# Kernel tuning notes

Hardware: AMD Instinct MI355X
Metric: run time of the kernel (lower is better)

The kernel has to match this reference:

```python
import jax, jax.numpy as jnp
import numpy as np

B, C, H, W, K, NCLASS = 8, 512, 96, 96, 32, 19
EPS = 1e-5


def setup_inputs() -> dict:
    key = jax.random.key(0)
    ks = jax.random.split(key, 10)
    return {
        "x": jax.random.normal(ks[0], (B, C, H, W), dtype=jnp.float32),
        "conv_w": jax.random.normal(ks[1], (C, C), dtype=jnp.float32) * (1.0 / np.sqrt(C)),
        "bn2_w": jax.random.uniform(ks[2], (C,), dtype=jnp.float32, minval=0.5, maxval=1.5),
        "bn2_b": jax.random.normal(ks[3], (C,), dtype=jnp.float32) * 0.1,
        "bn2_mean": jnp.zeros((C,), jnp.float32),
        "bn2_var": jnp.ones((C,), jnp.float32),
        "codewords": jax.random.normal(ks[4], (K, C), dtype=jnp.float32) * (1.0 / np.sqrt(C)),
        "scale": jax.random.uniform(ks[5], (K,), dtype=jnp.float32, minval=-1.0, maxval=0.0),
        "bn1_w": jax.random.uniform(ks[6], (K,), dtype=jnp.float32, minval=0.5, maxval=1.5),
        "bn1_b": jax.random.normal(ks[7], (K,), dtype=jnp.float32) * 0.1,
        "bn1_mean": jnp.zeros((K,), jnp.float32),
        "bn1_var": jnp.ones((K,), jnp.float32),
        "fc_w": jax.random.normal(ks[8], (C, C), dtype=jnp.float32) * (1.0 / np.sqrt(C)),
        "fc_b": jnp.zeros((C,), jnp.float32),
        "se_w": jax.random.normal(ks[9], (NCLASS, C), dtype=jnp.float32) * (1.0 / np.sqrt(C)),
        "se_b": jnp.zeros((NCLASS,), jnp.float32),
    }


def reference(x, conv_w, bn2_w, bn2_b, bn2_mean, bn2_var,
              codewords, scale, bn1_w, bn1_b, bn1_mean, bn1_var,
              fc_w, fc_b, se_w, se_b):
    # 1x1 conv (no bias) + BN2d (inference) + ReLU
    h = jnp.einsum('oc,bchw->bohw', conv_w, x)
    s2 = bn2_w / jnp.sqrt(bn2_var + EPS)
    h = jax.nn.relu(h * s2[None, :, None, None]
                    + (bn2_b - bn2_mean * s2)[None, :, None, None])

    # Encoding: soft assignment over K codewords
    X = h.reshape(B, C, H * W).transpose(0, 2, 1)       # (B, N, C)
    x2 = jnp.sum(X * X, axis=-1)                        # (B, N)
    c2 = jnp.sum(codewords * codewords, axis=-1)        # (K,)
    xc = jnp.einsum('bnd,kd->bnk', X, codewords)        # (B, N, K)
    sl = scale[None, None, :] * (x2[:, :, None] - 2.0 * xc + c2[None, None, :])
    A = jax.nn.softmax(sl, axis=-1)                     # (B, N, K)
    # E[b,k,d] = sum_n A[b,n,k] * (X[b,n,d] - codewords[k,d])
    E = (jnp.einsum('bnk,bnd->bkd', A, X)
         - jnp.sum(A, axis=1)[:, :, None] * codewords[None, :, :])  # (B, K, C)

    # BN1d over the K channel dim (inference) + ReLU + mean over K
    s1 = bn1_w / jnp.sqrt(bn1_var + EPS)
    E = jax.nn.relu(E * s1[None, :, None] + (bn1_b - bn1_mean * s1)[None, :, None])
    en = jnp.mean(E, axis=1)                            # (B, C)

    # SE-style gate
    gamma = jax.nn.sigmoid(en @ fc_w.T + fc_b)          # (B, C)
    out = jax.nn.relu(x + x * gamma[:, :, None, None])  # (B, C, H, W)
    se = en @ se_w.T + se_b                             # (B, NCLASS)
    return (out, se)
```

## Files before the change

### kernel.cpp

```cpp
#include <hip/hip_runtime.h>
#include <math.h>

#define EPSV 1e-5f

typedef __attribute__((ext_vector_type(8))) short short8;
typedef __attribute__((ext_vector_type(4))) float f32x4;

namespace {
constexpr int NB=8, C=512, NPIX=9216, K=32, NCLS=19;

constexpr size_t o_WB    = 0;
constexpr size_t o_CWB   = 131072;
constexpr size_t o_A2    = 139264;
constexpr size_t o_B2    = 139776;
constexpr size_t o_C2    = 140288;
constexpr size_t o_X2    = 140320;
constexpr size_t o_EW    = 214048;
constexpr size_t o_ACNT  = 345120;
constexpr size_t o_EN    = 345376;
constexpr size_t o_GAMMA = 349472;
constexpr size_t o_XT    = 353568;
constexpr size_t o_EPART = 19227936;
constexpr size_t WS_NEED = (o_EPART + (size_t)384*16384) * 4;

constexpr int NGRP   = 48;
constexpr int NTILE  = 3;
constexpr int ZERO_FL = NB*C*K + 256;
constexpr int CONV_LDS = (512*64 + 64*64)*2 + 64*4;
constexpr int ENC_LDS  = 36864*2 + 2304*2 + 64*4;
}

__device__ __forceinline__ ushort f2bf(float f){
  unsigned u = __float_as_uint(f);
  return (ushort)((u + 0x7FFFu + ((u>>16)&1u)) >> 16);
}
__device__ __forceinline__ float bf2f(ushort h){
  return __uint_as_float(((unsigned)h)<<16);
}

__global__ __launch_bounds__(256) void k_prep(
    const float* __restrict__ convw, ushort* __restrict__ Wb,
    const float* __restrict__ cw,    ushort* __restrict__ cwb,
    const float* __restrict__ bn2w, const float* __restrict__ bn2b,
    const float* __restrict__ bn2m, const float* __restrict__ bn2v,
    float* __restrict__ pa, float* __restrict__ pb, float* __restrict__ c2g,
    float* __restrict__ zero_dst)
{
  const int bid = blockIdx.x, t = threadIdx.x;
  if (bid < 136){
    const float* src = (bid < 128) ? convw : cw;
    ushort* dst      = (bid < 128) ? Wb    : cwb;
    const int base   = (bid < 128) ? bid   : (bid - 128);
    int i = (base*256 + t)*8;
    float4 a = *(const float4*)(src+i), b = *(const float4*)(src+i+4);
    uint4 o;
    o.x = f2bf(a.x) | ((unsigned)f2bf(a.y)<<16);
    o.y = f2bf(a.z) | ((unsigned)f2bf(a.w)<<16);
    o.z = f2bf(b.x) | ((unsigned)f2bf(b.y)<<16);
    o.w = f2bf(b.z) | ((unsigned)f2bf(b.w)<<16);
    *(uint4*)(dst+i) = o;
  } else if (bid == 136){
    for (int o = t; o < C; o += 256){
      float s = bn2w[o] * rsqrtf(bn2v[o] + EPSV);
      pa[o] = s;
      pb[o] = bn2b[o] - bn2m[o] * s;
    }
    int kk = t>>3, part = t&7;
    float s = 0.f;
    for (int c = part*64; c < part*64 + 64; c += 4){
      float4 w = *(const float4*)(cw + kk*512 + c);
      s += w.x*w.x + w.y*w.y + w.z*w.z + w.w*w.w;
    }
    s += __shfl_xor(s, 1);
    s += __shfl_xor(s, 2);
    s += __shfl_xor(s, 4);
    if (part == 0) c2g[kk] = s;
  } else {
    const int idx = ((bid - 137)*256 + t)*4;
    if (idx < ZERO_FL)
      *(float4*)(zero_dst + idx) = make_float4(0.f, 0.f, 0.f, 0.f);
  }
}

__global__ __launch_bounds__(256) void k_T(const float* __restrict__ x,
                                           ushort* __restrict__ xT){
  __shared__ float xs[64*68];
  const int bid = blockIdx.x;
  const int ct = bid & 7;
  const int nt = bid >> 3;
  const int b = nt / 144, ntl = nt % 144;
  const int c0 = ct*64, n0 = ntl*64;
  const int t = threadIdx.x;
  const float* src = x + ((size_t)b*C + c0)*NPIX + n0;
#pragma unroll
  for (int p = 0; p < 4; ++p){
    const int cr = p*16 + (t>>4);
    const int nc = (t&15)*4;
    *(float4*)(xs + cr*68 + nc) = *(const float4*)(src + (size_t)cr*NPIX + nc);
  }
  __syncthreads();
  const int nr = t>>2, ck = (t&3)*16;
  uint pk[8];
#pragma unroll
  for (int j = 0; j < 8; ++j){
    float f0 = xs[(ck + 2*j  )*68 + nr];
    float f1 = xs[(ck + 2*j+1)*68 + nr];
    pk[j] = (uint)f2bf(f0) | ((uint)f2bf(f1)<<16);
  }
  ushort* dst = xT + ((size_t)(b*NPIX + n0 + nr))*512 + c0 + ck;
  *(uint4*)(dst)   = make_uint4(pk[0],pk[1],pk[2],pk[3]);
  *(uint4*)(dst+8) = make_uint4(pk[4],pk[5],pk[6],pk[7]);
}

__global__ __launch_bounds__(256,2) void k_conv(
  const ushort* __restrict__ Wb, ushort* __restrict__ xT,
  const float* __restrict__ pA2, const float* __restrict__ pB2,
  float* __restrict__ x2g)
{
  extern __shared__ char smem[];
  ushort* As  = (ushort*)smem;
  ushort* Bs  = As + 512*64;
  float*  x2s = (float*)(Bs + 64*64);
  const int t = threadIdx.x;
  const int n0 = blockIdx.x * 64;
  const int wave = t>>6, lane = t&63;
  const int lg = lane>>4, l15 = lane&15;

  if (t < 64) x2s[t] = 0.f;

  f32x4 acc[8][4];
#pragma unroll
  for (int mi = 0; mi < 8; ++mi)
#pragma unroll
    for (int nj = 0; nj < 4; ++nj) acc[mi][nj] = (f32x4){0.f,0.f,0.f,0.f};

  const int srow = t>>3, sq = t&7;
  for (int s = 0; s < 8; ++s) {
    const int c0 = s*64;
    __syncthreads();
#pragma unroll
    for (int p = 0; p < 16; ++p) {
      const int r = p*32 + srow;
      uint4 v = *(const uint4*)(Wb + r*512 + c0 + sq*8);
      *(uint4*)(As + r*64 + (((sq ^ (r&7))&7)<<3)) = v;
    }
#pragma unroll
    for (int p = 0; p < 2; ++p) {
      const int r = p*32 + srow;
      uint4 v = *(const uint4*)(xT + (size_t)(n0+r)*512 + c0 + sq*8);
      *(uint4*)(Bs + r*64 + (((sq ^ (r&7))&7)<<3)) = v;
    }
    __syncthreads();
#pragma unroll
    for (int kk = 0; kk < 2; ++kk) {
      short8 af[8], bfv[4];
#pragma unroll
      for (int mi = 0; mi < 8; ++mi) {
        const int r = wave*128 + mi*16 + l15;
        af[mi] = *(const short8*)(As + r*64 + ((((kk*4+lg) ^ (r&7))&7)<<3));
      }
#pragma unroll
      for (int nj = 0; nj < 4; ++nj) {
        const int r = nj*16 + l15;
        bfv[nj] = *(const short8*)(Bs + r*64 + ((((kk*4+lg) ^ (r&7))&7)<<3));
      }
#pragma unroll
      for (int mi = 0; mi < 8; ++mi)
#pragma unroll
        for (int nj = 0; nj < 4; ++nj)
          acc[mi][nj] = __builtin_amdgcn_mfma_f32_16x16x32_bf16(af[mi], bfv[nj], acc[mi][nj], 0,0,0);
    }
  }

  float x2p[4] = {0.f,0.f,0.f,0.f};
#pragma unroll
  for (int mi = 0; mi < 8; ++mi) {
    const int ob = wave*128 + mi*16 + lg*4;
    const float4 sa = *(const float4*)(pA2 + ob);
    const float4 sb = *(const float4*)(pB2 + ob);
#pragma unroll
    for (int nj = 0; nj < 4; ++nj) {
      const int n = n0 + nj*16 + l15;
      f32x4 a = acc[mi][nj];
      float h0 = fmaxf(fmaf(a[0], sa.x, sb.x), 0.f);
      float h1 = fmaxf(fmaf(a[1], sa.y, sb.y), 0.f);
      float h2 = fmaxf(fmaf(a[2], sa.z, sb.z), 0.f);
      float h3 = fmaxf(fmaf(a[3], sa.w, sb.w), 0.f);
      x2p[nj] += h0*h0 + h1*h1 + h2*h2 + h3*h3;
      uint2 pk;
      pk.x = f2bf(h0) | ((unsigned)f2bf(h1)<<16);
      pk.y = f2bf(h2) | ((unsigned)f2bf(h3)<<16);
      *(uint2*)(xT + (size_t)n*512 + ob) = pk;
    }
  }
#pragma unroll
  for (int nj = 0; nj < 4; ++nj) {
    float v = x2p[nj];
    v += __shfl_xor(v, 16);
    v += __shfl_xor(v, 32);
    if (lg == 0) atomicAdd(&x2s[nj*16 + l15], v);
  }
  __syncthreads();
  if (t < 64) x2g[n0 + t] = x2s[t];
}

__global__ __launch_bounds__(256,2) void k_enc2(
  const ushort* __restrict__ hT, const float* __restrict__ x2g,
  const ushort* __restrict__ cwb, const float* __restrict__ scale,
  const float* __restrict__ c2g, float* __restrict__ Ebase,
  float* __restrict__ Acnt, int atomicE)
{
  extern __shared__ ushort sm16[];
  ushort* hbuf = sm16;
  ushort* Pl   = sm16 + 36864;
  float*  x2s  = (float*)(sm16 + 36864 + 2304);

  const int t = threadIdx.x, bid = blockIdx.x;
  const int wave = t>>6, lane = t&63, lg = lane>>4, l15 = lane&15;
  const int b = bid / NGRP;

  float sc[2][4], cv[2][4];
#pragma unroll
  for (int f=0; f<2; ++f)
#pragma unroll
    for (int i=0; i<4; ++i){
      int k = f*16 + lg*4 + i;
      sc[f][i] = scale[k];
      cv[f][i] = c2g[k];
    }

  f32x4 Eacc[2][8];
#pragma unroll
  for (int f=0; f<2; ++f)
#pragma unroll
    for (int nf=0; nf<8; ++nf) Eacc[f][nf] = (f32x4){0.f,0.f,0.f,0.f};
  float acs[2][4] = {{0.f,0.f,0.f,0.f},{0.f,0.f,0.f,0.f}};

  for (int tt = 0; tt < NTILE; ++tt){
    const int tile = bid*NTILE + tt;
    const size_t n0 = (size_t)tile*64;
    __syncthreads();
    {
      const int px = t>>2, cq = t&3;
      const ushort* src = hT + (n0+px)*512 + cq*128;
      ushort* dst = hbuf + px*520 + cq*128;
#pragma unroll
      for (int i=0; i<16; ++i)
        *(uint4*)(dst + i*8) = *(const uint4*)(src + i*8);
    }
    if (t < 64) x2s[t] = x2g[n0 + t];
    __syncthreads();

    f32x4 xacc[2];
    xacc[0] = (f32x4){0.f,0.f,0.f,0.f};
    xacc[1] = (f32x4){0.f,0.f,0.f,0.f};
    {
      const ushort* hrow  = hbuf + (wave*16 + l15)*520 + lg*8;
      const ushort* arow0 = cwb + (l15)*512 + lg*8;
      const ushort* arow1 = cwb + (16 + l15)*512 + lg*8;
#pragma unroll
      for (int s = 0; s < 16; ++s){
        short8 bfr = *(const short8*)(hrow  + s*32);
        short8 a0  = *(const short8*)(arow0 + s*32);
        short8 a1  = *(const short8*)(arow1 + s*32);
        xacc[0] = __builtin_amdgcn_mfma_f32_16x16x32_bf16(a0, bfr, xacc[0], 0,0,0);
        xacc[1] = __builtin_amdgcn_mfma_f32_16x16x32_bf16(a1, bfr, xacc[1], 0,0,0);
      }
    }
    const float x2v = x2s[wave*16 + l15];
    float sl[2][4];
    float mx = -1e30f;
#pragma unroll
    for (int f=0; f<2; ++f)
#pragma unroll
      for (int i=0; i<4; ++i){
        sl[f][i] = sc[f][i]*(x2v - 2.f*xacc[f][i] + cv[f][i]);
        mx = fmaxf(mx, sl[f][i]);
      }
    mx = fmaxf(mx, __shfl_xor(mx, 16));
    mx = fmaxf(mx, __shfl_xor(mx, 32));
    float pv[2][4];
    float ssum = 0.f;
#pragma unroll
    for (int f=0; f<2; ++f)
#pragma unroll
      for (int i=0; i<4; ++i){
        pv[f][i] = __expf(sl[f][i] - mx);
        ssum += pv[f][i];
      }
    ssum += __shfl_xor(ssum, 16);
    ssum += __shfl_xor(ssum, 32);
    const float inv = 1.f/ssum;
#pragma unroll
    for (int f=0; f<2; ++f)
#pragma unroll
      for (int i=0; i<4; ++i){
        float p = pv[f][i]*inv;
        ushort pb = f2bf(p);
        acs[f][i] += bf2f(pb);
        Pl[(f*16 + lg*4 + i)*72 + wave*16 + l15] = pb;
      }
    uint4 treg[16];
    {
      const ushort* src = hbuf + lane*520 + wave*128;
#pragma unroll
      for (int i=0; i<16; ++i) treg[i] = *(const uint4*)(src + i*8);
    }
    __syncthreads();
    {
      ushort* dstT = hbuf + (size_t)(wave*128)*72 + lane;
#pragma unroll
      for (int i=0; i<16; ++i){
        uint4 v = treg[i];
#pragma unroll
        for (int w2=0; w2<4; ++w2){
          unsigned word = (&v.x)[w2];
          dstT[(i*8 + w2*2    )*72] = (ushort)(word & 0xFFFFu);
          dstT[(i*8 + w2*2 + 1)*72] = (ushort)(word >> 16);
        }
      }
    }
    __syncthreads();
    short8 pa[2][2];
#pragma unroll
    for (int f=0; f<2; ++f)
#pragma unroll
      for (int ks=0; ks<2; ++ks)
        pa[f][ks] = *(const short8*)(Pl + (f*16 + l15)*72 + ks*32 + lg*8);
#pragma unroll
    for (int nf=0; nf<8; ++nf){
      const ushort* brow = hbuf + (size_t)(wave*128 + nf*16 + l15)*72 + lg*8;
      short8 b0 = *(const short8*)(brow);
      short8 b1 = *(const short8*)(brow + 32);
      Eacc[0][nf] = __builtin_amdgcn_mfma_f32_16x16x32_bf16(pa[0][0], b0, Eacc[0][nf], 0,0,0);
      Eacc[0][nf] = __builtin_amdgcn_mfma_f32_16x16x32_bf16(pa[0][1], b1, Eacc[0][nf], 0,0,0);
      Eacc[1][nf] = __builtin_amdgcn_mfma_f32_16x16x32_bf16(pa[1][0], b0, Eacc[1][nf], 0,0,0);
      Eacc[1][nf] = __builtin_amdgcn_mfma_f32_16x16x32_bf16(pa[1][1], b1, Eacc[1][nf], 0,0,0);
    }
  }

  if (atomicE){
    float* pbase = Ebase + (size_t)b*16384;
#pragma unroll
    for (int f=0; f<2; ++f)
#pragma unroll
      for (int nf=0; nf<8; ++nf){
        const int c = wave*128 + nf*16 + l15;
        float* p = pbase + (size_t)c*32 + f*16 + lg*4;
        atomicAdd(p+0, Eacc[f][nf][0]);
        atomicAdd(p+1, Eacc[f][nf][1]);
        atomicAdd(p+2, Eacc[f][nf][2]);
        atomicAdd(p+3, Eacc[f][nf][3]);
      }
  } else {
    float* pbase = Ebase + (size_t)bid*16384;
#pragma unroll
    for (int f=0; f<2; ++f)
#pragma unroll
      for (int nf=0; nf<8; ++nf){
        const int c = wave*128 + nf*16 + l15;
        *(f32x4*)(pbase + (size_t)c*32 + f*16 + lg*4) = Eacc[f][nf];
      }
  }
#pragma unroll
  for (int f=0; f<2; ++f)
#pragma unroll
    for (int i=0; i<4; ++i){
      float v = acs[f][i];
      v += __shfl_xor(v, 1);
      v += __shfl_xor(v, 2);
      v += __shfl_xor(v, 4);
      v += __shfl_xor(v, 8);
      if (l15 == 0) atomicAdd(&Acnt[b*32 + f*16 + lg*4 + i], v);
    }
}

__global__ __launch_bounds__(256) void k_en2(
    const float* __restrict__ Epart, const float* __restrict__ EwAtomic,
    const float* __restrict__ Acnt, const float* __restrict__ cw,
    const float* __restrict__ bn1w, const float* __restrict__ bn1b,
    const float* __restrict__ bn1m, const float* __restrict__ bn1v,
    float* __restrict__ en, int useAtomic)
{
  const int b = blockIdx.x >> 6;
  const int cchunk = blockIdx.x & 63;
  const int t = threadIdx.x;
  const int c_local = t >> 5, k = t & 31;
  const int c = cchunk*8 + c_local;

  float acc = 0.f;
  if (!useAtomic){
    const float* base = Epart + (size_t)b*NGRP*16384 + cchunk*256 + t;
    for (int g = 0; g < NGRP; ++g)
      acc += base[(size_t)g*16384];
  } else {
    acc = EwAtomic[(size_t)b*16384 + (size_t)c*32 + k];
  }
  float s1 = bn1w[k]*rsqrtf(bn1v[k]+EPSV);
  float t1 = bn1b[k] - bn1m[k]*s1;
  float e = acc - Acnt[b*32 + k]*cw[(size_t)k*512 + c];
  float v = fmaxf(fmaf(e, s1, t1), 0.f);
  v += __shfl_xor(v, 1);
  v += __shfl_xor(v, 2);
  v += __shfl_xor(v, 4);
  v += __shfl_xor(v, 8);
  v += __shfl_xor(v, 16);
  if (k == 0) en[(size_t)b*512 + c] = v*(1.f/32.f);
}

__global__ __launch_bounds__(512) void k_gate(
    const float* __restrict__ en, const float* __restrict__ fcw,
    const float* __restrict__ fcb, const float* __restrict__ sew,
    const float* __restrict__ seb, float* __restrict__ gamma,
    float* __restrict__ se_out)
{
    __shared__ float es[C];
    const int b = blockIdx.x;
    es[threadIdx.x] = en[(size_t)b * C + threadIdx.x];
    __syncthreads();
    {
        const int c = threadIdx.x;
        float z = fcb[c];
        const float* wr = fcw + (size_t)c * C;
        for (int i = 0; i < C; i += 4) {
            const float4 w = *(const float4*)(wr + i);
            z += w.x * es[i] + w.y * es[i + 1] + w.z * es[i + 2] + w.w * es[i + 3];
        }
        gamma[(size_t)b * C + c] = 1.f / (1.f + expf(-z));
    }
    if (threadIdx.x < NCLS * 8) {
        const int j = threadIdx.x >> 3, lane = threadIdx.x & 7;
        float p = 0.f;
        const float* swr = sew + (size_t)j * C;
        for (int i = lane * 64; i < lane * 64 + 64; i += 4) {
            const float4 w = *(const float4*)(swr + i);
            p += w.x * es[i] + w.y * es[i + 1] + w.z * es[i + 2] + w.w * es[i + 3];
        }
        p += __shfl_xor(p, 1);
        p += __shfl_xor(p, 2);
        p += __shfl_xor(p, 4);
        if (lane == 0) se_out[b * NCLS + j] = p + seb[j];
    }
}

__global__ __launch_bounds__(256) void k_out(
    const float* __restrict__ x, const float* __restrict__ gamma,
    float* __restrict__ out)
{
    const int total4 = NB * C * NPIX / 4;
    for (int i = blockIdx.x * blockDim.x + threadIdx.x; i < total4;
         i += gridDim.x * blockDim.x) {
        const int flat = i * 4;
        const int bc = flat / NPIX;
        const float gsc = 1.f + gamma[bc];
        float4 v = *(const float4*)(x + flat);
        v.x = fmaxf(v.x * gsc, 0.f);
        v.y = fmaxf(v.y * gsc, 0.f);
        v.z = fmaxf(v.z * gsc, 0.f);
        v.w = fmaxf(v.w * gsc, 0.f);
        *(float4*)(out + flat) = v;
    }
}

extern "C" void kernel_launch(void* const* d_in, const int* in_sizes, int n_in,
                              void* d_out, int out_size, void* d_ws, size_t ws_size,
                              hipStream_t stream)
{
    const float* x     = (const float*)d_in[0];
    const float* convw = (const float*)d_in[1];
    const float* bn2w  = (const float*)d_in[2];
    const float* bn2b  = (const float*)d_in[3];
    const float* bn2m  = (const float*)d_in[4];
    const float* bn2v  = (const float*)d_in[5];
    const float* cw    = (const float*)d_in[6];
    const float* scale = (const float*)d_in[7];
    const float* bn1w  = (const float*)d_in[8];
    const float* bn1b  = (const float*)d_in[9];
    const float* bn1m  = (const float*)d_in[10];
    const float* bn1v  = (const float*)d_in[11];
    const float* fcw   = (const float*)d_in[12];
    const float* fcb   = (const float*)d_in[13];
    const float* sew   = (const float*)d_in[14];
    const float* seb   = (const float*)d_in[15];

    float* ws = (float*)d_ws;
    float* out = (float*)d_out;
    float* se_out = out + (size_t)NB * C * NPIX;

    ushort* Wb  = (ushort*)(ws + o_WB);
    ushort* cwb = (ushort*)(ws + o_CWB);
    ushort* xT  = (ushort*)(ws + o_XT);

    const bool use_part = ws_size >= WS_NEED;
    float* Ebase = use_part ? (ws + o_EPART) : (ws + o_EW);
    const int useAtomic = use_part ? 0 : 1;

    (void)hipFuncSetAttribute((const void*)k_conv,
                              hipFuncAttributeMaxDynamicSharedMemorySize, CONV_LDS);
    (void)hipFuncSetAttribute((const void*)k_enc2,
                              hipFuncAttributeMaxDynamicSharedMemorySize, ENC_LDS);

    k_prep<<<266, 256, 0, stream>>>(convw, Wb, cw, cwb,
                                    bn2w, bn2b, bn2m, bn2v,
                                    ws + o_A2, ws + o_B2, ws + o_C2, ws + o_EW);
    k_T<<<9216, 256, 0, stream>>>(x, xT);
    k_conv<<<1152, 256, CONV_LDS, stream>>>(Wb, xT, ws + o_A2, ws + o_B2, ws + o_X2);
    k_enc2<<<384, 256, ENC_LDS, stream>>>(xT, ws + o_X2, cwb, scale, ws + o_C2,
                                          Ebase, ws + o_ACNT, useAtomic);
    k_en2<<<512, 256, 0, stream>>>(Ebase, ws + o_EW, ws + o_ACNT, cw,
                                   bn1w, bn1b, bn1m, bn1v, ws + o_EN, useAtomic);
    k_gate<<<8, 512, 0, stream>>>(ws + o_EN, fcw, fcb, sew, seb,
                                  ws + o_GAMMA, se_out);
    k_out<<<2048, 256, 0, stream>>>(x, ws + o_GAMMA, out);
}
```

Baseline: 293.8 us.

## Share conv weight tile across two pixel tiles per 512-thread block

The 1x1 conv kernel now runs 512 threads per block, with two 256-thread halves each computing a 64-pixel tile while sharing one LDS copy of the 512x64 weight slice. This halves the number of weight loads from global memory into LDS per pixel processed. The per-pixel squared-norm reduction now uses global atomics directly instead of an LDS buffer, so the prep kernel gains extra blocks to zero that buffer. The costs are more global atomics and a larger block, whose LDS and register footprint may limit occupancy.

Result: slower. 310.1 us (+5.5%).

```diff
diff --git a/kernel.cpp b/kernel.cpp
--- a/kernel.cpp
+++ b/kernel.cpp
@@ -25,8 +25,9 @@
 
 constexpr int NGRP   = 48;
 constexpr int NTILE  = 3;
-constexpr int ZERO_FL = NB*C*K + 256;
-constexpr int CONV_LDS = (512*64 + 64*64)*2 + 64*4;
+constexpr int ZERO_FL  = NB*C*K + 256;
+constexpr int ZERO2_FL = 73728;
+constexpr int CONV_LDS = (512*64 + 64*64 + 64*64)*2;
 constexpr int ENC_LDS  = 36864*2 + 2304*2 + 64*4;
 }
 
@@ -44,7 +45,7 @@
     const float* __restrict__ bn2w, const float* __restrict__ bn2b,
     const float* __restrict__ bn2m, const float* __restrict__ bn2v,
     float* __restrict__ pa, float* __restrict__ pb, float* __restrict__ c2g,
-    float* __restrict__ zero_dst)
+    float* __restrict__ zero_dst, float* __restrict__ zero2_dst)
 {
   const int bid = blockIdx.x, t = threadIdx.x;
   if (bid < 136){
@@ -75,10 +76,14 @@
     s += __shfl_xor(s, 2);
     s += __shfl_xor(s, 4);
     if (part == 0) c2g[kk] = s;
-  } else {
+  } else if (bid < 266){
     const int idx = ((bid - 137)*256 + t)*4;
     if (idx < ZERO_FL)
       *(float4*)(zero_dst + idx) = make_float4(0.f, 0.f, 0.f, 0.f);
+  } else {
+    const int idx = ((bid - 266)*256 + t)*4;
+    if (idx < ZERO2_FL)
+      *(float4*)(zero2_dst + idx) = make_float4(0.f, 0.f, 0.f, 0.f);
   }
 }
 
@@ -112,43 +117,46 @@
   *(uint4*)(dst+8) = make_uint4(pk[4],pk[5],pk[6],pk[7]);
 }
 
-__global__ __launch_bounds__(256,2) void k_conv(
+__global__ __launch_bounds__(512,2) void k_conv(
   const ushort* __restrict__ Wb, ushort* __restrict__ xT,
   const float* __restrict__ pA2, const float* __restrict__ pB2,
   float* __restrict__ x2g)
 {
   extern __shared__ char smem[];
-  ushort* As  = (ushort*)smem;
-  ushort* Bs  = As + 512*64;
-  float*  x2s = (float*)(Bs + 64*64);
+  ushort* As = (ushort*)smem;
+  ushort* Bs = As + 512*64 + (threadIdx.x >= 256 ? 64*64 : 0);
+
   const int t = threadIdx.x;
-  const int n0 = blockIdx.x * 64;
-  const int wave = t>>6, lane = t&63;
+  const int h = t >> 8;
+  const int u = t & 255;
+  const int n0 = blockIdx.x * 128 + h*64;
+  const int wave = u>>6, lane = t&63;
   const int lg = lane>>4, l15 = lane&15;
 
-  if (t < 64) x2s[t] = 0.f;
-
   f32x4 acc[8][4];
 #pragma unroll
   for (int mi = 0; mi < 8; ++mi)
 #pragma unroll
     for (int nj = 0; nj < 4; ++nj) acc[mi][nj] = (f32x4){0.f,0.f,0.f,0.f};
 
-  const int srow = t>>3, sq = t&7;
+  const int srowA = t>>3, sqA = t&7;
+  const int srowB = u>>3, sqB = u&7;
   for (int s = 0; s < 8; ++s) {
     const int c0 = s*64;
     __syncthreads();
 #pragma unroll
-    for (int p = 0; p < 16; ++p) {
-      const int r = p*32 + srow;
-      uint4 v = *(const uint4*)(Wb + r*512 + c0 + sq*8);
-      *(uint4*)(As + r*64 + (((sq ^ (r&7))&7)<<3)) = v;
-    }
-#pragma unroll
-    for (int p = 0; p < 2; ++p) {
-      const int r = p*32 + srow;
-      uint4 v = *(const uint4*)(xT + (size_t)(n0+r)*512 + c0 + sq*8);
-      *(uint4*)(Bs + r*64 + (((sq ^ (r&7))&7)<<3)) = v;
+    for (int p = 0; p < 8; ++p) {
+      const int r = p*64 + srowA;
+      uint4 v = *(const uint4*)(Wb + r*512 + c0 + sqA*8);
+      *(uint4*)(As + r*64 + (((sqA ^ (r&7))&7)<<3)) = v;
+    }
+    {
+      const int r = srowB;
+      uint4 v0 = *(const uint4*)(xT + (size_t)(n0+r)*512 + c0 + sqB*8);
+      *(uint4*)(Bs + r*64 + (((sqB ^ (r&7))&7)<<3)) = v0;
+      const int r2 = 32 + srowB;
+      uint4 v1 = *(const uint4*)(xT + (size_t)(n0+r2)*512 + c0 + sqB*8);
+      *(uint4*)(Bs + r2*64 + (((sqB ^ (r2&7))&7)<<3)) = v1;
     }
     __syncthreads();
 #pragma unroll
@@ -198,10 +206,8 @@
     float v = x2p[nj];
     v += __shfl_xor(v, 16);
     v += __shfl_xor(v, 32);
-    if (lg == 0) atomicAdd(&x2s[nj*16 + l15], v);
-  }
-  __syncthreads();
-  if (t < 64) x2g[n0 + t] = x2s[t];
+    if (lg == 0) atomicAdd(&x2g[n0 + nj*16 + l15], v);
+  }
 }
 
 __global__ __launch_bounds__(256,2) void k_enc2(
@@ -500,11 +506,12 @@
     (void)hipFuncSetAttribute((const void*)k_enc2,
                               hipFuncAttributeMaxDynamicSharedMemorySize, ENC_LDS);
 
-    k_prep<<<266, 256, 0, stream>>>(convw, Wb, cw, cwb,
+    k_prep<<<338, 256, 0, stream>>>(convw, Wb, cw, cwb,
                                     bn2w, bn2b, bn2m, bn2v,
-                                    ws + o_A2, ws + o_B2, ws + o_C2, ws + o_EW);
+                                    ws + o_A2, ws + o_B2, ws + o_C2,
+                                    ws + o_EW, ws + o_X2);
     k_T<<<9216, 256, 0, stream>>>(x, xT);
-    k_conv<<<1152, 256, CONV_LDS, stream>>>(Wb, xT, ws + o_A2, ws + o_B2, ws + o_X2);
+    k_conv<<<576, 512, CONV_LDS, stream>>>(Wb, xT, ws + o_A2, ws + o_B2, ws + o_X2);
     k_enc2<<<384, 256, ENC_LDS, stream>>>(xT, ws + o_X2, cwb, scale, ws + o_C2,
                                           Ebase, ws + o_ACNT, useAtomic);
     k_en2<<<512, 256, 0, stream>>>(Ebase, ws + o_EW, ws + o_ACNT, cw,
```
